# Kernel optimization log

Measured on AMD Instinct MI355X. Metric: run time of the kernel, lower is better.

Reference implementation:

```python
import jax, jax.numpy as jnp
import numpy as np

N = 1024      # num nodes
E = 16384     # num edges
P = 8192      # num query pairs
HD1 = 64      # hidden_dim_1
HD2 = 64      # hidden_dim_2
VOCAB = 1000  # max_x + 1
EPS = 1e-5


def gcn_conv(x, W, b, src, dst, n):
    # PyG GCNConv: h = D^{-1/2} (A + I) D^{-1/2} (x @ W) + b
    h = x @ W
    loop = jnp.arange(n)
    s = jnp.concatenate([src, loop])
    d = jnp.concatenate([dst, loop])
    deg = jnp.zeros((n,), h.dtype).at[d].add(1.0)
    dis = jax.lax.rsqrt(deg)  # deg >= 1 due to self-loops
    norm = dis[s] * dis[d]
    out = jnp.zeros_like(h).at[d].add(norm[:, None] * h[s])
    return out + b


def graph_norm(x, w, b, alpha):
    # PyG GraphNorm with a single graph: stats over node dim (axis 0)
    mean = jnp.mean(x, axis=0, keepdims=True)
    sh = x - alpha * mean
    var = jnp.mean(sh * sh, axis=0, keepdims=True)
    return w * sh / jnp.sqrt(var + EPS) + b


def _forward(x_ids, ei, pos, emb, gW0, gb0, gnw0, gnb0, gna0, gW1, gb1,
             gnw1, gnb1, gna1, m1W, m1b, m2W, m2b, m3W, m3b,
             gn3w, gn3b, gn3a, ldW, ldb):
    n = x_ids.shape[0]
    src, dst = ei[0], ei[1]
    x = emb[x_ids]                                            # [n, HD1]
    # 1-WL: two GCNConv -> GraphNorm -> ReLU blocks
    x = jax.nn.relu(graph_norm(gcn_conv(x, gW0, gb0, src, dst, n), gnw0, gnb0, gna0))
    x = jax.nn.relu(graph_norm(gcn_conv(x, gW1, gb1, src, dst, n), gnw1, gnb1, gna1))
    # O(n^2) outer product: X[i,j] = x[i] * x[j]
    X = x[:, None, :] * x[None, :, :]                         # [n, n, HD1]
    eim = jnp.zeros((n, n), x.dtype).at[src, dst].set(1.0)    # adjacency indicator
    # add_chan = eye(n) @ eim = eim
    X = jnp.concatenate([X, eim[:, :, None]], axis=-1)        # [n, n, HD1+1]
    # 2-FWL refinement (layer2 = 1)
    x1 = jax.nn.relu(X @ m1W + m1b)                           # [n, n, HD2]
    x2 = jax.nn.relu(X @ m2W + m2b)                           # [n, n, HD2]
    prod = jnp.einsum('ikc,kjc->ijc', x1, x2)                 # per-channel bmm
    X = jnp.concatenate([X, prod], axis=-1)                   # [n, n, HD1+1+HD2]
    X = jax.nn.relu(graph_norm(X @ m3W + m3b, gn3w, gn3b, gn3a))
    # symmetric mul-pool then gather query pairs
    X = X * jnp.transpose(X, (1, 0, 2))                       # [n, n, HD2]
    feat = X[pos[:, 0], pos[:, 1]]                            # [P, HD2]
    return feat @ ldW + ldb                                   # [P, 1]


def setup_inputs() -> dict:
    key = jax.random.key(0)
    ks = jax.random.split(key, 12)
    sc = lambda k, s: jax.random.normal(k, s, jnp.float32) * 0.05
    d = {}
    d['x_ids'] = jax.random.randint(ks[0], (N,), 0, VOCAB)
    d['ei'] = jax.random.randint(ks[1], (2, E), 0, N)
    d['pos'] = jax.random.randint(ks[2], (P, 2), 0, N)
    d['emb'] = sc(ks[3], (VOCAB, HD1))
    d['gW0'] = sc(ks[4], (HD1, HD1)); d['gb0'] = jnp.zeros((HD1,), jnp.float32)
    d['gnw0'] = jnp.ones((HD1,), jnp.float32); d['gnb0'] = jnp.zeros((HD1,), jnp.float32); d['gna0'] = jnp.ones((HD1,), jnp.float32)
    d['gW1'] = sc(ks[5], (HD1, HD1)); d['gb1'] = jnp.zeros((HD1,), jnp.float32)
    d['gnw1'] = jnp.ones((HD1,), jnp.float32); d['gnb1'] = jnp.zeros((HD1,), jnp.float32); d['gna1'] = jnp.ones((HD1,), jnp.float32)
    d['m1W'] = sc(ks[6], (HD1 + 1, HD2)); d['m1b'] = jnp.zeros((HD2,), jnp.float32)
    d['m2W'] = sc(ks[7], (HD1 + 1, HD2)); d['m2b'] = jnp.zeros((HD2,), jnp.float32)
    d['m3W'] = sc(ks[8], (HD2 + HD1 + 1, HD2)); d['m3b'] = jnp.zeros((HD2,), jnp.float32)
    d['gn3w'] = jnp.ones((HD2,), jnp.float32); d['gn3b'] = jnp.zeros((HD2,), jnp.float32); d['gn3a'] = jnp.ones((HD2,), jnp.float32)
    d['ldW'] = sc(ks[9], (HD2, 1)); d['ldb'] = jnp.zeros((1,), jnp.float32)
    return d


def reference(x_ids, ei, pos, emb, gW0, gb0, gnw0, gnb0, gna0, gW1, gb1,
              gnw1, gnb1, gna1, m1W, m1b, m2W, m2b, m3W, m3b,
              gn3w, gn3b, gn3a, ldW, ldb):
    return _forward(x_ids, ei, pos, emb, gW0, gb0, gnw0, gnb0, gna0, gW1, gb1,
                    gnw1, gnb1, gna1, m1W, m1b, m2W, m2b, m3W, m3b,
                    gn3w, gn3b, gn3a, ldW, ldb)
```

## Files before the change

### kernel.cpp

```cpp
#include <hip/hip_runtime.h>


typedef unsigned short u16;
typedef unsigned int u32;

#define DI static __device__ __forceinline__

DI float bf2f(u16 u) { union { u32 i; float f; } v; v.i = ((u32)u) << 16; return v.f; }
DI u16 f2bf(float f) {
  union { float f; u32 i; } v; v.f = f;
  u32 u = v.i;
  return (u16)((u + 0x7fffu + ((u >> 16) & 1u)) >> 16);
}

typedef __bf16 bf16x8 __attribute__((ext_vector_type(8)));
typedef float f32x4 __attribute__((ext_vector_type(4)));

#define MFMA16(a, b, c) __builtin_amdgcn_mfma_f32_16x16x32_bf16((a), (b), (c), 0, 0, 0)

typedef const __attribute__((address_space(1))) u32* gas1;
typedef __attribute__((address_space(3))) u32* las3;


__global__ void k_setup(const int* __restrict__ xids, const float* __restrict__ emb,
                        float* __restrict__ xf, float* __restrict__ deg,
                        u32* __restrict__ eimu) {
  int g = blockIdx.x * 256 + threadIdx.x;
  if (g < 262144) eimu[g] = 0u;
  if (g < 1024) deg[g] = 1.0f;
  if (g < 65536) {
    int i = g >> 6, d = g & 63;
    xf[g] = emb[xids[i] * 64 + d];
  }
}

__global__ void k_edges(const int* __restrict__ ei, float* __restrict__ deg,
                        unsigned char* __restrict__ eim) {
  int e = blockIdx.x * 256 + threadIdx.x;
  if (e < 16384) {
    int s = ei[e], d = ei[16384 + e];
    atomicAdd(&deg[d], 1.0f);
    eim[s * 1024 + d] = 1;
  }
}

__global__ void k_gemm_node(const float* __restrict__ xf, const float* __restrict__ W,
                            const float* __restrict__ gb, const float* __restrict__ deg,
                            float* __restrict__ h, float* __restrict__ agg) {
  __shared__ float xrow[64];
  int i = blockIdx.x, c = threadIdx.x;
  xrow[c] = xf[i * 64 + c];
  __syncthreads();
  float s = 0.f;
#pragma unroll
  for (int d = 0; d < 64; ++d) s += xrow[d] * W[d * 64 + c];
  h[i * 64 + c] = s;
  agg[i * 64 + c] = s / deg[i] + gb[c];
}

__global__ void k_agg(const int* __restrict__ ei, const float* __restrict__ deg,
                      const float* __restrict__ h, float* __restrict__ agg) {
  int g = blockIdx.x * 256 + threadIdx.x;
  int e = g >> 6, c = g & 63;
  int s = ei[e], d = ei[16384 + e];
  float nrm = rsqrtf(deg[s]) * rsqrtf(deg[d]);
  atomicAdd(&agg[d * 64 + c], nrm * h[s * 64 + c]);
}

__global__ void k_gnorm(const float* __restrict__ agg, const float* __restrict__ gw,
                        const float* __restrict__ gbb, const float* __restrict__ ga,
                        float* __restrict__ xf, u16* __restrict__ xb, int last) {
  int c = blockIdx.x, t = threadIdx.x;
  float s = 0.f, ss = 0.f;
  for (int i = t; i < 1024; i += 256) {
    float v = agg[i * 64 + c];
    s += v; ss += v * v;
  }
  __shared__ float Ls[256], Lss[256];
  Ls[t] = s; Lss[t] = ss;
  __syncthreads();
  for (int off = 128; off > 0; off >>= 1) {
    if (t < off) { Ls[t] += Ls[t + off]; Lss[t] += Lss[t + off]; }
    __syncthreads();
  }
  float m = Ls[0] * (1.f / 1024.f);
  float a = ga[c];
  float var = Lss[0] * (1.f / 1024.f) - (2.f * a - a * a) * m * m;
  float sc = gw[c] * rsqrtf(fmaxf(var, 0.f) + 1e-5f);
  float bb = gbb[c];
  for (int i = t; i < 1024; i += 256) {
    float v = agg[i * 64 + c];
    float y = fmaxf(sc * (v - a * m) + bb, 0.f);
    xf[i * 64 + c] = y;
    if (last) xb[i * 64 + c] = f2bf(y);
  }
}

__global__ __launch_bounds__(256, 2) void k_build12(
    const u16* __restrict__ xbg, const unsigned char* __restrict__ eim,
    const float* __restrict__ m1W, const float* __restrict__ m1b,
    const float* __restrict__ m2W, const float* __restrict__ m2b,
    u16* __restrict__ x1tg, u16* __restrict__ x2tg, int cbase) {
  __shared__ u16 As[128 * 80];
  __shared__ u16 Bs[128 * 80];
  __shared__ u16 Cs[64 * 140];
  __shared__ unsigned char El[128 * 132];
  __shared__ float wsc[64];
  int b = blockIdx.x;
  int cg = b & 3;
  int rest = b >> 2;
  int which = rest >> 6;
  int t6 = rest & 63;
  int rbase = (t6 >> 3) * 128, sbase = (t6 & 7) * 128;
  const float* W = which ? m2W : m1W;
  const float* bias = which ? m2b : m1b;
  u16* outg = which ? x2tg : x1tg;
  int t = threadIdx.x;
  {
    int row = t >> 1, half = t & 1;
    const u32* gB = (const u32*)(xbg + (sbase + row) * 64 + half * 32);
    u32* dstB = (u32*)&Bs[row * 80 + half * 32];
#pragma unroll
    for (int k = 0; k < 16; ++k) dstB[k] = gB[k];
    int ab = which ? sbase : rbase;
    int bb = which ? rbase : sbase;
    const u32* gE = (const u32*)(eim + (size_t)(ab + row) * 1024 + bb + half * 64);
    u32* dstE = (u32*)&El[row * 132 + half * 64];
#pragma unroll
    for (int k = 0; k < 16; ++k) dstE[k] = gE[k];
  }
  int lane = t & 63, w = t >> 6;
  int q = lane >> 4, r = lane & 15;
  int wr = w >> 1, wc = w & 1;
  for (int ci = 0; ci < 4; ++ci) {
    int cl = cg * 4 + ci;
    int c = cbase + cl;
    if (t < 64) wsc[t] = W[t * 64 + c];
    __syncthreads();
    {
      int row = t >> 1, half = t & 1;
      const u32* ga = (const u32*)(xbg + (rbase + row) * 64 + half * 32);
      u32* dstA = (u32*)&As[row * 80 + half * 32];
#pragma unroll
      for (int k = 0; k < 16; ++k) {
        u32 u = ga[k];
        float f0 = bf2f((u16)(u & 0xffffu)) * wsc[half * 32 + 2 * k];
        float f1 = bf2f((u16)(u >> 16)) * wsc[half * 32 + 2 * k + 1];
        dstA[k] = (u32)f2bf(f0) | ((u32)f2bf(f1) << 16);
      }
    }
    __syncthreads();
    f32x4 z4 = {0.f, 0.f, 0.f, 0.f};
    f32x4 acc[4][4];
#pragma unroll
    for (int mi = 0; mi < 4; ++mi)
#pragma unroll
      for (int ni = 0; ni < 4; ++ni) acc[mi][ni] = z4;
#pragma unroll
    for (int ks = 0; ks < 2; ++ks) {
      bf16x8 af[4], bfr[4];
#pragma unroll
      for (int mi = 0; mi < 4; ++mi)
        af[mi] = *(const bf16x8*)&As[(wr * 64 + mi * 16 + r) * 80 + ks * 32 + q * 8];
#pragma unroll
      for (int ni = 0; ni < 4; ++ni)
        bfr[ni] = *(const bf16x8*)&Bs[(wc * 64 + ni * 16 + r) * 80 + ks * 32 + q * 8];
#pragma unroll
      for (int mi = 0; mi < 4; ++mi)
#pragma unroll
        for (int ni = 0; ni < 4; ++ni) acc[mi][ni] = MFMA16(af[mi], bfr[ni], acc[mi][ni]);
    }
    float w64 = W[64 * 64 + c];
    float bsv = bias[c];
#pragma unroll
    for (int mi = 0; mi < 4; ++mi) {
#pragma unroll
      for (int ni = 0; ni < 4; ++ni) {
        int col = wc * 64 + ni * 16 + r;
#pragma unroll
        for (int tt = 0; tt < 4; ++tt) {
          int row2 = wr * 64 + mi * 16 + q * 4 + tt;
          float e = (float)(which ? El[col * 132 + row2] : El[row2 * 132 + col]);
          acc[mi][ni][tt] = fmaxf(acc[mi][ni][tt] + e * w64 + bsv, 0.f);
        }
      }
    }
    u16* outp = outg + (size_t)cl * 1048576;
#pragma unroll
    for (int p = 0; p < 2; ++p) {
      __syncthreads();
      if (wr == p) {
#pragma unroll
        for (int mi = 0; mi < 4; ++mi)
#pragma unroll
          for (int ni = 0; ni < 4; ++ni) {
            int col = wc * 64 + ni * 16 + r;
#pragma unroll
            for (int tt = 0; tt < 4; ++tt) {
              int lrow = mi * 16 + q * 4 + tt;
              Cs[lrow * 140 + col] = f2bf(acc[mi][ni][tt]);
            }
          }
      }
      __syncthreads();
      {
        int rl = t >> 4, ch = t & 15;
#pragma unroll
        for (int it = 0; it < 4; ++it) {
          int row = it * 16 + rl;
          uint4 v = *(const uint4*)&Cs[row * 140 + ch * 8];
          *(uint4*)(outp + (size_t)(rbase + p * 64 + row) * 1024 + sbase + ch * 8) = v;
        }
      }
    }
  }
}

__global__ __launch_bounds__(256, 4) void k_prodgemm(
    const u16* __restrict__ x1tg, const u16* __restrict__ x2tg,
    u16* __restrict__ prod, int cbase) {
  __shared__ u16 pool[17408];
  int b = blockIdx.x;
  int cl = (b & 7) + ((b >> 9) << 3);
  int tile = (b >> 3) & 63;
  int i0 = (tile >> 3) * 128, j0 = (tile & 7) * 128;
  const u16* Ap = x1tg + (size_t)cl * 1048576;
  const u16* Bp = x2tg + (size_t)cl * 1048576;
  u16* Pp = prod + (size_t)(cbase + cl) * 1048576;
  int t = threadIdx.x, lane = t & 63, w = t >> 6;
  int q = lane >> 4, r = lane & 15;
  int wr = w >> 1, wc = w & 1;
  int lrow = lane >> 3, lcol = (lane & 7) * 8;
  f32x4 z4 = {0.f, 0.f, 0.f, 0.f};
  f32x4 acc[4][4];
#pragma unroll
  for (int mi = 0; mi < 4; ++mi)
#pragma unroll
    for (int ni = 0; ni < 4; ++ni) acc[mi][ni] = z4;
  for (int kk = 0; kk < 1024; kk += 64) {
    __syncthreads();
#pragma unroll
    for (int s8 = 0; s8 < 4; ++s8) {
      int rowbase = w * 32 + s8 * 8;
      int grow = rowbase + lrow;
      __builtin_amdgcn_global_load_lds(
          (gas1)(Ap + (size_t)(i0 + grow) * 1024 + kk + lcol),
          (las3)&pool[rowbase * 64], 16, 0, 0);
      __builtin_amdgcn_global_load_lds(
          (gas1)(Bp + (size_t)(j0 + grow) * 1024 + kk + lcol),
          (las3)&pool[8192 + rowbase * 64], 16, 0, 0);
    }
    __syncthreads();
#pragma unroll
    for (int ks = 0; ks < 2; ++ks) {
      bf16x8 af[4], bfr[4];
#pragma unroll
      for (int mi = 0; mi < 4; ++mi)
        af[mi] = *(const bf16x8*)&pool[(wr * 64 + mi * 16 + r) * 64 + ks * 32 + q * 8];
#pragma unroll
      for (int ni = 0; ni < 4; ++ni)
        bfr[ni] = *(const bf16x8*)&pool[8192 + (wc * 64 + ni * 16 + r) * 64 + ks * 32 + q * 8];
#pragma unroll
      for (int mi = 0; mi < 4; ++mi)
#pragma unroll
        for (int ni = 0; ni < 4; ++ni) acc[mi][ni] = MFMA16(af[mi], bfr[ni], acc[mi][ni]);
    }
  }
  __syncthreads();
#pragma unroll
  for (int mi = 0; mi < 4; ++mi)
#pragma unroll
    for (int ni = 0; ni < 4; ++ni) {
      int col = wc * 64 + ni * 16 + r;
#pragma unroll
      for (int tt = 0; tt < 4; ++tt) {
        int row2 = wr * 64 + mi * 16 + q * 4 + tt;
        pool[row2 * 136 + col] = f2bf(acc[mi][ni][tt]);
      }
    }
  __syncthreads();
  {
    int rseg = t >> 4, cseg = t & 15;
#pragma unroll
    for (int it = 0; it < 8; ++it) {
      int row = it * 16 + rseg;
      uint4 v = *(const uint4*)&pool[row * 136 + cseg * 8];
      *(uint4*)(Pp + (size_t)(i0 + row) * 1024 + j0 + cseg * 8) = v;
    }
  }
}

__global__ __launch_bounds__(256, 3) void k_buildT(
    const u16* __restrict__ xbg, const unsigned char* __restrict__ eim,
    u16* PT, const float* __restrict__ m3W, const float* __restrict__ m3b,
    float* __restrict__ S, float* __restrict__ SS) {
  __shared__ __align__(16) u16 A[64 * 136];
  __shared__ u16 Wt[64 * 136];
  __shared__ u16 scratch[64 * 66];
  __shared__ __align__(16) u16 stg[64 * 72];
  __shared__ unsigned char eimrow[1024];
  int bx = blockIdx.x;
  int i = bx >> 1, bj = bx & 1;
  int jbase = bj * 512;
  int t = threadIdx.x, lane = t & 63, w = t >> 6;
  int q = lane >> 4, r = lane & 15;
  {
    int zidx = i * 256 + t;
    if (zidx < 65536) { S[zidx] = 0.f; SS[zidx] = 0.f; }
  }
  ((u32*)eimrow)[t] = ((const u32*)(eim + (size_t)i * 1024))[t];
  {
    int row = t >> 1, half = t & 1;
    int rsrc = row < 64 ? row : row + 1;
    float xsc = (row < 64) ? bf2f(xbg[i * 64 + row]) : 1.f;
    const float4* gw = (const float4*)(m3W + rsrc * 64 + half * 32);
#pragma unroll
    for (int k = 0; k < 8; ++k) {
      float4 f = gw[k];
      Wt[(half * 32 + 4 * k + 0) * 136 + row] = f2bf(f.x * xsc);
      Wt[(half * 32 + 4 * k + 1) * 136 + row] = f2bf(f.y * xsc);
      Wt[(half * 32 + 4 * k + 2) * 136 + row] = f2bf(f.z * xsc);
      Wt[(half * 32 + 4 * k + 3) * 136 + row] = f2bf(f.w * xsc);
    }
  }
  float w64c[4], b3c[4];
#pragma unroll
  for (int ni = 0; ni < 4; ++ni) {
    int cc = ni * 16 + r;
    w64c[ni] = m3W[64 * 64 + cc];
    b3c[ni] = m3b[cc];
  }
  int p4 = t >> 2, q4 = t & 3;
  uint4 pva, pvb, xva, xvb;
  {
    const uint4* gp = (const uint4*)(PT + (size_t)p4 * 1048576 + (size_t)i * 1024 + jbase + q4 * 16);
    pva = gp[0]; pvb = gp[1];
    const uint4* gx = (const uint4*)(xbg + (jbase + p4) * 64 + q4 * 16);
    xva = gx[0]; xvb = gx[1];
  }
  for (int jc8 = 0; jc8 < 8; ++jc8) {
    int j0 = jbase + jc8 * 64;
    asm volatile("s_waitcnt lgkmcnt(0)" ::: "memory");
    __builtin_amdgcn_s_barrier();
    asm volatile("" ::: "memory");
    {
      u32* sw = (u32*)&scratch[p4 * 66 + q4 * 16];
      sw[0] = pva.x; sw[1] = pva.y; sw[2] = pva.z; sw[3] = pva.w;
      sw[4] = pvb.x; sw[5] = pvb.y; sw[6] = pvb.z; sw[7] = pvb.w;
      *(uint4*)&A[p4 * 136 + q4 * 16] = xva;
      *(uint4*)&A[p4 * 136 + q4 * 16 + 8] = xvb;
    }
    if (jc8 < 7) {
      const uint4* gp = (const uint4*)(PT + (size_t)p4 * 1048576 + (size_t)i * 1024 + (j0 + 64) + q4 * 16);
      pva = gp[0]; pvb = gp[1];
      const uint4* gx = (const uint4*)(xbg + (j0 + 64 + p4) * 64 + q4 * 16);
      xva = gx[0]; xvb = gx[1];
    }
    if (jc8 > 0) {
      int pl = t >> 3, off = (t & 7) * 8;
#pragma unroll
      for (int k = 0; k < 2; ++k) {
        int plane = k * 32 + pl;
        uint4 v = *(const uint4*)&stg[plane * 72 + off];
        *(uint4*)(PT + (size_t)plane * 1048576 + (size_t)i * 1024 + (j0 - 64) + off) = v;
      }
    }
    asm volatile("s_waitcnt lgkmcnt(0)" ::: "memory");
    __builtin_amdgcn_s_barrier();
    asm volatile("" ::: "memory");
#pragma unroll
    for (int jj2 = 0; jj2 < 8; ++jj2) {
      int jr = w * 16 + jj2 * 2;
      u32 two = *(const u32*)&scratch[lane * 66 + jr];
      A[jr * 136 + 64 + lane] = (u16)(two & 0xffffu);
      A[(jr + 1) * 136 + 64 + lane] = (u16)(two >> 16);
    }
    asm volatile("s_waitcnt lgkmcnt(0)" ::: "memory");
    __builtin_amdgcn_s_barrier();
    asm volatile("" ::: "memory");
    f32x4 z4 = {0.f, 0.f, 0.f, 0.f};
    f32x4 acc[4];
#pragma unroll
    for (int ni = 0; ni < 4; ++ni) acc[ni] = z4;
#pragma unroll
    for (int ks = 0; ks < 4; ++ks) {
      bf16x8 af, bfr[4];
      af = *(const bf16x8*)&A[(w * 16 + r) * 136 + ks * 32 + q * 8];
#pragma unroll
      for (int ni = 0; ni < 4; ++ni)
        bfr[ni] = *(const bf16x8*)&Wt[(ni * 16 + r) * 136 + ks * 32 + q * 8];
#pragma unroll
      for (int ni = 0; ni < 4; ++ni) acc[ni] = MFMA16(af, bfr[ni], acc[ni]);
    }
#pragma unroll
    for (int tt = 0; tt < 4; ++tt) {
      int jj = w * 16 + q * 4 + tt;
      float ev = (float)eimrow[j0 + jj];
#pragma unroll
      for (int ni = 0; ni < 4; ++ni)
        acc[ni][tt] = acc[ni][tt] + ev * w64c[ni] + b3c[ni];
    }
#pragma unroll
    for (int ni = 0; ni < 4; ++ni) {
      int cc = ni * 16 + r;
      u32 lo = (u32)f2bf(acc[ni][0]) | ((u32)f2bf(acc[ni][1]) << 16);
      u32 hi = (u32)f2bf(acc[ni][2]) | ((u32)f2bf(acc[ni][3]) << 16);
      uint2 vv; vv.x = lo; vv.y = hi;
      *(uint2*)&stg[cc * 72 + w * 16 + q * 4] = vv;
    }
  }
  asm volatile("s_waitcnt lgkmcnt(0)" ::: "memory");
  __builtin_amdgcn_s_barrier();
  asm volatile("" ::: "memory");
  {
    int pl = t >> 3, off = (t & 7) * 8;
#pragma unroll
    for (int k = 0; k < 2; ++k) {
      int plane = k * 32 + pl;
      uint4 v = *(const uint4*)&stg[plane * 72 + off];
      *(uint4*)(PT + (size_t)plane * 1048576 + (size_t)i * 1024 + (jbase + 448) + off) = v;
    }
  }
}

__global__ void k_stats(const u16* __restrict__ Tg, float* __restrict__ S,
                        float* __restrict__ SS) {
  int b = blockIdx.x;
  int c = b >> 3, ic = b & 7;
  int t = threadIdx.x;
  const u16* base = Tg + (size_t)c * 1048576 + (size_t)ic * 131072 + t * 4;
  float s0 = 0.f, s1 = 0.f, s2 = 0.f, s3 = 0.f;
  float q0 = 0.f, q1 = 0.f, q2 = 0.f, q3 = 0.f;
  for (int ii = 0; ii < 128; ++ii) {
    uint2 u = *(const uint2*)(base + (size_t)ii * 1024);
    float v0 = bf2f((u16)(u.x & 0xffffu)), v1 = bf2f((u16)(u.x >> 16));
    float v2 = bf2f((u16)(u.y & 0xffffu)), v3 = bf2f((u16)(u.y >> 16));
    s0 += v0; q0 += v0 * v0;
    s1 += v1; q1 += v1 * v1;
    s2 += v2; q2 += v2 * v2;
    s3 += v3; q3 += v3 * v3;
  }
  int base2 = c * 1024 + t * 4;
  atomicAdd(&S[base2 + 0], s0);
  atomicAdd(&S[base2 + 1], s1);
  atomicAdd(&S[base2 + 2], s2);
  atomicAdd(&S[base2 + 3], s3);
  atomicAdd(&SS[base2 + 0], q0);
  atomicAdd(&SS[base2 + 1], q1);
  atomicAdd(&SS[base2 + 2], q2);
  atomicAdd(&SS[base2 + 3], q3);
}

__global__ void k_statsfin(const float* __restrict__ S, const float* __restrict__ SS,
                           const float* __restrict__ gn3w, const float* __restrict__ gn3b,
                           const float* __restrict__ gn3a,
                           float* __restrict__ normA, float* __restrict__ normB) {
  int idx = blockIdx.x * 256 + threadIdx.x;
  int c = idx & 63, j = idx >> 6;
  float sum = S[c * 1024 + j];
  float ssum = SS[c * 1024 + j];
  float m = sum * (1.f / 1024.f);
  float a = gn3a[c];
  float var = ssum * (1.f / 1024.f) - (2.f * a - a * a) * m * m;
  float sc = gn3w[c] * rsqrtf(fmaxf(var, 0.f) + 1e-5f);
  normA[idx] = sc;
  normB[idx] = gn3b[c] - sc * a * m;
}

__global__ void k_final(const u16* __restrict__ Tg, const float* __restrict__ normA,
                        const float* __restrict__ normB, const int* __restrict__ pos,
                        const float* __restrict__ ldW, const float* __restrict__ ldb,
                        float* __restrict__ out) {
  int t = threadIdx.x, w = t >> 6, lane = t & 63;
  int p = blockIdx.x * 4 + w;
  int i = pos[2 * p], j = pos[2 * p + 1];
  float t1 = bf2f(Tg[(size_t)lane * 1048576 + (size_t)i * 1024 + j]);
  float y1 = fmaxf(normA[j * 64 + lane] * t1 + normB[j * 64 + lane], 0.f);
  float t2 = bf2f(Tg[(size_t)lane * 1048576 + (size_t)j * 1024 + i]);
  float y2 = fmaxf(normA[i * 64 + lane] * t2 + normB[i * 64 + lane], 0.f);
  float z = y1 * y2 * ldW[lane];
#pragma unroll
  for (int off = 32; off > 0; off >>= 1) z += __shfl_down(z, off, 64);
  if (lane == 0) out[p] = z + ldb[0];
}

extern "C" void kernel_launch(void* const* d_in, const int* in_sizes, int n_in,
                              void* d_out, int out_size, void* d_ws, size_t ws_size,
                              hipStream_t stream) {
  const int* xids   = (const int*)d_in[0];
  const int* ei     = (const int*)d_in[1];
  const int* pos    = (const int*)d_in[2];
  const float* emb  = (const float*)d_in[3];
  const float* gW0  = (const float*)d_in[4];
  const float* gb0  = (const float*)d_in[5];
  const float* gnw0 = (const float*)d_in[6];
  const float* gnb0 = (const float*)d_in[7];
  const float* gna0 = (const float*)d_in[8];
  const float* gW1  = (const float*)d_in[9];
  const float* gb1  = (const float*)d_in[10];
  const float* gnw1 = (const float*)d_in[11];
  const float* gnb1 = (const float*)d_in[12];
  const float* gna1 = (const float*)d_in[13];
  const float* m1W  = (const float*)d_in[14];
  const float* m1b  = (const float*)d_in[15];
  const float* m2W  = (const float*)d_in[16];
  const float* m2b  = (const float*)d_in[17];
  const float* m3W  = (const float*)d_in[18];
  const float* m3b  = (const float*)d_in[19];
  const float* gn3w = (const float*)d_in[20];
  const float* gn3b = (const float*)d_in[21];
  const float* gn3a = (const float*)d_in[22];
  const float* ldW  = (const float*)d_in[23];
  const float* ldb  = (const float*)d_in[24];

  char* ws = (char*)d_ws;
  float* xf   = (float*)(ws + 0);
  float* h    = (float*)(ws + 262144);
  float* agg  = (float*)(ws + 524288);
  float* deg  = (float*)(ws + 786432);
  u16*   xb   = (u16*)(ws + 790528);
  unsigned char* eim = (unsigned char*)(ws + 921600);
  float* normA = (float*)(ws + 1970176);
  float* normB = (float*)(ws + 2232320);
  u16* x1tg = (u16*)(ws + 2494464);
  u16* x2tg = (u16*)(ws + 36048896);
  u16* prod = (u16*)(ws + 69603328);
  float* Sp  = (float*)x1tg;
  float* SSp = Sp + 65536;
  float* out = (float*)d_out;

  k_setup<<<1024, 256, 0, stream>>>(xids, emb, xf, deg, (u32*)eim);
  k_edges<<<64, 256, 0, stream>>>(ei, deg, eim);
  k_gemm_node<<<1024, 64, 0, stream>>>(xf, gW0, gb0, deg, h, agg);
  k_agg<<<4096, 256, 0, stream>>>(ei, deg, h, agg);
  k_gnorm<<<64, 256, 0, stream>>>(agg, gnw0, gnb0, gna0, xf, xb, 0);
  k_gemm_node<<<1024, 64, 0, stream>>>(xf, gW1, gb1, deg, h, agg);
  k_agg<<<4096, 256, 0, stream>>>(ei, deg, h, agg);
  k_gnorm<<<64, 256, 0, stream>>>(agg, gnw1, gnb1, gna1, xf, xb, 1);
  for (int g = 0; g < 4; ++g) {
    k_build12<<<512, 256, 0, stream>>>(xb, eim, m1W, m1b, m2W, m2b, x1tg, x2tg, g * 16);
    k_prodgemm<<<1024, 256, 0, stream>>>(x1tg, x2tg, prod, g * 16);
  }
  k_buildT<<<2048, 256, 0, stream>>>(xb, eim, prod, m3W, m3b, Sp, SSp);
  k_stats<<<512, 256, 0, stream>>>(prod, Sp, SSp);
  k_statsfin<<<256, 256, 0, stream>>>(Sp, SSp, gn3w, gn3b, gn3a, normA, normB);
  k_final<<<2048, 256, 0, stream>>>(prod, normA, normB, pos, ldW, ldb, out);
}
```

Before: 502.5 us.

## Double-buffer LDS tiles in prodgemm to overlap global loads with MFMA

The per-channel bmm kernel now splits its LDS pool into two 32-wide K buffers. It issues the next tile's global_load_lds before computing on the current one, with explicit vmcnt waits and raw s_barriers in place of __syncthreads. The goal is to hide global load latency behind the MFMA work. The cost is more barrier iterations at half the K depth each, plus manual waitcnt bookkeeping that has to match the number of loads in flight.

New measurement: 499.6 us (median of 3 runs). Within noise of the previous version (-0.6%).

```diff
diff --git a/kernel.cpp b/kernel.cpp
--- a/kernel.cpp
+++ b/kernel.cpp
@@ -230,42 +230,62 @@
   int t = threadIdx.x, lane = t & 63, w = t >> 6;
   int q = lane >> 4, r = lane & 15;
   int wr = w >> 1, wc = w & 1;
-  int lrow = lane >> 3, lcol = (lane & 7) * 8;
+  int srow = lane >> 2, scol = (lane & 3) * 8;
+
+#define PSTAGE(KT)                                                          \
+  {                                                                         \
+    int pb_ = (KT) & 1;                                                     \
+    int kk_ = (KT) * 32;                                                    \
+    _Pragma("unroll")                                                       \
+    for (int s = 0; s < 2; ++s) {                                           \
+      int rowb = w * 32 + s * 16;                                           \
+      __builtin_amdgcn_global_load_lds(                                     \
+          (gas1)(Ap + (size_t)(i0 + rowb + srow) * 1024 + kk_ + scol),      \
+          (las3)(pool + pb_ * 8192 + rowb * 32), 16, 0, 0);                 \
+      __builtin_amdgcn_global_load_lds(                                     \
+          (gas1)(Bp + (size_t)(j0 + rowb + srow) * 1024 + kk_ + scol),      \
+          (las3)(pool + pb_ * 8192 + 4096 + rowb * 32), 16, 0, 0);          \
+    }                                                                       \
+  }
+
   f32x4 z4 = {0.f, 0.f, 0.f, 0.f};
   f32x4 acc[4][4];
 #pragma unroll
   for (int mi = 0; mi < 4; ++mi)
 #pragma unroll
     for (int ni = 0; ni < 4; ++ni) acc[mi][ni] = z4;
-  for (int kk = 0; kk < 1024; kk += 64) {
-    __syncthreads();
-#pragma unroll
-    for (int s8 = 0; s8 < 4; ++s8) {
-      int rowbase = w * 32 + s8 * 8;
-      int grow = rowbase + lrow;
-      __builtin_amdgcn_global_load_lds(
-          (gas1)(Ap + (size_t)(i0 + grow) * 1024 + kk + lcol),
-          (las3)&pool[rowbase * 64], 16, 0, 0);
-      __builtin_amdgcn_global_load_lds(
-          (gas1)(Bp + (size_t)(j0 + grow) * 1024 + kk + lcol),
-          (las3)&pool[8192 + rowbase * 64], 16, 0, 0);
-    }
-    __syncthreads();
-#pragma unroll
-    for (int ks = 0; ks < 2; ++ks) {
+
+  PSTAGE(0);
+#pragma unroll 2
+  for (int kt = 0; kt < 32; ++kt) {
+    int pb = kt & 1;
+    if (kt < 31) {
+      PSTAGE(kt + 1);
+      asm volatile("s_waitcnt vmcnt(4)" ::: "memory");
+    } else {
+      asm volatile("s_waitcnt vmcnt(0)" ::: "memory");
+    }
+    __builtin_amdgcn_s_barrier();
+    asm volatile("" ::: "memory");
+    {
       bf16x8 af[4], bfr[4];
 #pragma unroll
       for (int mi = 0; mi < 4; ++mi)
-        af[mi] = *(const bf16x8*)&pool[(wr * 64 + mi * 16 + r) * 64 + ks * 32 + q * 8];
+        af[mi] = *(const bf16x8*)&pool[pb * 8192 + (wr * 64 + mi * 16 + r) * 32 + q * 8];
 #pragma unroll
       for (int ni = 0; ni < 4; ++ni)
-        bfr[ni] = *(const bf16x8*)&pool[8192 + (wc * 64 + ni * 16 + r) * 64 + ks * 32 + q * 8];
+        bfr[ni] = *(const bf16x8*)&pool[pb * 8192 + 4096 + (wc * 64 + ni * 16 + r) * 32 + q * 8];
 #pragma unroll
       for (int mi = 0; mi < 4; ++mi)
 #pragma unroll
         for (int ni = 0; ni < 4; ++ni) acc[mi][ni] = MFMA16(af[mi], bfr[ni], acc[mi][ni]);
     }
-  }
+    asm volatile("s_waitcnt lgkmcnt(0)" ::: "memory");
+    __builtin_amdgcn_s_barrier();
+    asm volatile("" ::: "memory");
+  }
+#undef PSTAGE
+
   __syncthreads();
 #pragma unroll
   for (int mi = 0; mi < 4; ++mi)
```
